# Performance work log

Measured on AMD Instinct MI355X. Metric: run time of the kernel, lower is better.

Reference implementation:

```python
import jax, jax.numpy as jnp
import numpy as np

N_NODES = 100000
AVG_DEG = 16
D_IN, D_HID, D_OUT = 128, 128, 64


def setup_inputs() -> dict:
    key = jax.random.key(0)
    k_x, k_w1, k_w2 = jax.random.split(key, 3)
    rng = np.random.default_rng(0)
    # random adjacency edges + self-loops (I + A)
    src = rng.integers(0, N_NODES, N_NODES * AVG_DEG)
    dst = rng.integers(0, N_NODES, N_NODES * AVG_DEG)
    loops = np.arange(N_NODES)
    src = np.concatenate([src, loops]).astype(np.int32)
    dst = np.concatenate([dst, loops]).astype(np.int32)
    # symmetric normalization D^{-1/2} (I+A) D^{-1/2}; deg = row sums of I+A
    deg = np.bincount(src, minlength=N_NODES).astype(np.float32)
    val = (1.0 / np.sqrt(deg[src] * deg[dst])).astype(np.float32)
    return {
        "x": jax.random.normal(k_x, (N_NODES, D_IN), dtype=jnp.float32),
        "W1": jax.random.normal(k_w1, (D_IN, D_HID), dtype=jnp.float32),
        "W2": jax.random.normal(k_w2, (D_HID, D_OUT), dtype=jnp.float32),
        "edge_src": jnp.asarray(src),
        "edge_dst": jnp.asarray(dst),
        "edge_val": jnp.asarray(val),
    }


def _gcn_layer(x, W, src, dst, val, n):
    xw = x @ W                               # dense GEMM: [N, d_out]
    msg = val[:, None] * xw[dst]             # gather along edges: [E, d_out]
    return jax.ops.segment_sum(msg, src, num_segments=n)  # A_hat @ (XW)


def reference(x, W1, W2, edge_src, edge_dst, edge_val):
    n = x.shape[0]
    h = jax.nn.relu(_gcn_layer(x, W1, edge_src, edge_dst, edge_val, n))
    h = jax.nn.relu(_gcn_layer(h, W2, edge_src, edge_dst, edge_val, n))
    return jax.nn.softmax(h, axis=-1)
```

## Files before the change

### kernel.cpp

```cpp
#include <hip/hip_runtime.h>
#include <hip/hip_fp16.h>
#include <math.h>

#define DHID 128
#define DOUT 64
#define EPB 4096
#define BUCK_SH 8

typedef _Float16 half8 __attribute__((ext_vector_type(8)));
typedef float f32x4 __attribute__((ext_vector_type(4)));

static inline size_t align_up(size_t v, size_t a) { return (v + a - 1) / a * a; }


__global__ __launch_bounds__(256) void k_bincount(const int* __restrict__ src, int* __restrict__ dir,
                                                  int* __restrict__ btot, int E, int nbuck, int nblka) {
    __shared__ int hist[512];
    int tid = threadIdx.x;
    for (int i = tid; i < nbuck; i += 256) hist[i] = 0;
    __syncthreads();
    int e0 = blockIdx.x * EPB;
    #pragma unroll
    for (int j = 0; j < EPB / 256; ++j) {
        int e = e0 + tid + j * 256;
        if (e < E) atomicAdd(&hist[src[e] >> BUCK_SH], 1);
    }
    __syncthreads();
    for (int i = tid; i < nbuck; i += 256) {
        int c = hist[i];
        dir[i * nblka + blockIdx.x] = c;
        if (c) atomicAdd(&btot[i], c);
    }
}

__global__ __launch_bounds__(256) void k_dirscan(int* __restrict__ dir, const int* __restrict__ btot,
                                                 int* __restrict__ bucketbase, int* __restrict__ off,
                                                 int n, int nbuck, int nblka, int E) {
    __shared__ int h[512], s4[128], redb[256];
    int tid = threadIdx.x, b = blockIdx.x;
    int s = 0;
    for (int i = tid; i < b; i += 256) s += btot[i];
    redb[tid] = s; __syncthreads();
    #pragma unroll
    for (int d = 128; d > 0; d >>= 1) {
        if (tid < d) redb[tid] += redb[tid + d];
        __syncthreads();
    }
    int base = redb[0];
    if (tid == 0) {
        bucketbase[b] = base;
        if (b == 0) off[n] = E;
        if (b == nbuck - 1) bucketbase[nbuck] = E;
    }
    for (int j = tid; j < nblka; j += 256) h[j] = dir[b * nblka + j];
    __syncthreads();
    int nq = (nblka + 3) >> 2;
    if (tid < nq) {
        int t = 0;
        #pragma unroll
        for (int j = 0; j < 4; ++j) { int idx = tid * 4 + j; if (idx < nblka) t += h[idx]; }
        s4[tid] = t;
    }
    __syncthreads();
    if (tid == 0) { int run = 0; for (int i = 0; i < nq; ++i) { int t = s4[i]; s4[i] = run; run += t; } }
    __syncthreads();
    if (tid < nq) {
        int run = s4[tid] + base;
        #pragma unroll
        for (int j = 0; j < 4; ++j) {
            int idx = tid * 4 + j;
            if (idx < nblka) { int t = h[idx]; dir[b * nblka + idx] = run; run += t; }
        }
    }
}

__global__ __launch_bounds__(256) void k_binwrite(const int* __restrict__ src, const int* __restrict__ dst,
                                                  const float* __restrict__ val, const int* __restrict__ dir,
                                                  int2* __restrict__ ctmp, int E, int nbuck, int nblka) {
    __shared__ int cur[512];
    int tid = threadIdx.x, blk = blockIdx.x;
    for (int i = tid; i < nbuck; i += 256) cur[i] = dir[i * nblka + blk];
    __syncthreads();
    int e0 = blk * EPB;
    #pragma unroll
    for (int j = 0; j < EPB / 256; ++j) {
        int e = e0 + tid + j * 256;
        if (e < E) {
            int s = src[e];
            int bk = s >> BUCK_SH;
            int p = atomicAdd(&cur[bk], 1);
            ctmp[p] = make_int2(((s & 255) << 17) | dst[e], __float_as_int(val[e]));
        }
    }
}

__global__ __launch_bounds__(256) void k_csrify(const int* __restrict__ bucketbase,
                                                const int2* __restrict__ ctmp, int2* __restrict__ cpair,
                                                int* __restrict__ off, int n) {
    __shared__ int h[256], loff[256], cur[256], s4[64];
    int tid = threadIdx.x, b = blockIdx.x;
    int base = bucketbase[b];
    int cnt = bucketbase[b + 1] - base;
    h[tid] = 0;
    __syncthreads();
    for (int i = tid; i < cnt; i += 256) atomicAdd(&h[ctmp[base + i].x >> 17], 1);
    __syncthreads();
    if (tid < 64) {
        int s = 0;
        #pragma unroll
        for (int j = 0; j < 4; ++j) s += h[tid * 4 + j];
        s4[tid] = s;
    }
    __syncthreads();
    if (tid == 0) { int run = 0; for (int i = 0; i < 64; ++i) { int t = s4[i]; s4[i] = run; run += t; } }
    __syncthreads();
    if (tid < 64) {
        int run = s4[tid];
        #pragma unroll
        for (int j = 0; j < 4; ++j) { int idx = tid * 4 + j; loff[idx] = run; run += h[idx]; }
    }
    __syncthreads();
    int node0 = b << BUCK_SH;
    int nodes_b = n - node0; if (nodes_b > 256) nodes_b = 256;
    if (tid < nodes_b) off[node0 + tid] = base + loff[tid];
    cur[tid] = loff[tid];
    __syncthreads();
    for (int i = tid; i < cnt; i += 256) {
        int2 v = ctmp[base + i];
        int sl = v.x >> 17;
        int p = atomicAdd(&cur[sl], 1);
        cpair[base + p] = make_int2(v.x & 0x1FFFF, v.y);
    }
}

__global__ __launch_bounds__(256) void k_wprep(const float* __restrict__ W1, const float* __restrict__ W2,
                                               _Float16* __restrict__ Wt1, _Float16* __restrict__ Wt2,
                                               int* __restrict__ btot, int nbuck) {
    int b = blockIdx.x, tid = threadIdx.x;
    int gid = b * 256 + tid;
    if (gid < nbuck) btot[gid] = 0;
    if (b < 64) {
        int m = b * 256 + tid;
        int c = m >> 7, k = m & 127;
        Wt1[m] = (_Float16)W1[(size_t)k * 128 + c];
    } else {
        int m = (b - 64) * 256 + tid;
        int c = m >> 7, k = m & 127;
        Wt2[m] = (_Float16)W2[(size_t)k * 64 + c];
    }
}

__global__ __launch_bounds__(256) void k_gemm1(const float* __restrict__ x, const _Float16* __restrict__ Wt1,
                                               __half* __restrict__ xw, int n) {
    __shared__ _Float16 Ws[128 * 128];
    int tid = threadIdx.x;
    int row0 = blockIdx.x * 64;

    #pragma unroll
    for (int m0 = 0; m0 < 2048; m0 += 256) {
        int m = tid + m0;
        int c = m >> 4, kq = m & 15;
        uint4 v = *(const uint4*)(Wt1 + (size_t)m * 8);
        int byte = (c * 256 + kq * 16) ^ ((c & 7) << 4);
        *(uint4*)((char*)Ws + byte) = v;
    }
    __syncthreads();

    int lane = tid & 63;
    int wid = tid >> 6;
    int rg = row0 + wid * 16 + (lane & 15); if (rg >= n) rg = n - 1;
    int kgrp = (lane >> 4) * 8;

    f32x4 acc[8];
    #pragma unroll
    for (int t = 0; t < 8; ++t) acc[t] = (f32x4){0.f, 0.f, 0.f, 0.f};

    #pragma unroll
    for (int kk = 0; kk < 128; kk += 32) {
        int ks = kk + kgrp;
        const float4* xp = (const float4*)(x + (size_t)rg * 128 + ks);
        float4 f0 = xp[0], f1 = xp[1];
        half8 a;
        a[0] = (_Float16)f0.x; a[1] = (_Float16)f0.y; a[2] = (_Float16)f0.z; a[3] = (_Float16)f0.w;
        a[4] = (_Float16)f1.x; a[5] = (_Float16)f1.y; a[6] = (_Float16)f1.z; a[7] = (_Float16)f1.w;
        #pragma unroll
        for (int t = 0; t < 8; ++t) {
            int c = t * 16 + (lane & 15);
            int bbyte = (c * 256 + ks * 2) ^ ((c & 7) << 4);
            half8 b = *(const half8*)((const char*)Ws + bbyte);
            acc[t] = __builtin_amdgcn_mfma_f32_16x16x32_f16(a, b, acc[t], 0, 0, 0);
        }
    }

    #pragma unroll
    for (int t = 0; t < 8; ++t) {
        int c = t * 16 + (lane & 15);
        #pragma unroll
        for (int j = 0; j < 4; ++j) {
            int rs = row0 + wid * 16 + (lane >> 4) * 4 + j;
            if (rs < n) xw[(size_t)rs * 128 + c] = __float2half(acc[t][j]);
        }
    }
}

__global__ __launch_bounds__(256) void k_gemm2(const __half* __restrict__ h1, const _Float16* __restrict__ Wt2,
                                               __half* __restrict__ hw, int n) {
    __shared__ _Float16 Ws[64 * 128];
    int tid = threadIdx.x;
    int row0 = blockIdx.x * 64;

    #pragma unroll
    for (int m0 = 0; m0 < 1024; m0 += 256) {
        int m = tid + m0;
        int c = m >> 4, kq = m & 15;
        uint4 v = *(const uint4*)(Wt2 + (size_t)m * 8);
        int byte = (c * 256 + kq * 16) ^ ((c & 7) << 4);
        *(uint4*)((char*)Ws + byte) = v;
    }
    __syncthreads();

    int lane = tid & 63;
    int wid = tid >> 6;
    int rg = row0 + wid * 16 + (lane & 15); if (rg >= n) rg = n - 1;
    int kgrp = (lane >> 4) * 8;

    f32x4 acc[4];
    #pragma unroll
    for (int t = 0; t < 4; ++t) acc[t] = (f32x4){0.f, 0.f, 0.f, 0.f};

    #pragma unroll
    for (int kk = 0; kk < 128; kk += 32) {
        int ks = kk + kgrp;
        half8 a = *(const half8*)((const void*)(h1 + (size_t)rg * 128 + ks));
        #pragma unroll
        for (int t = 0; t < 4; ++t) {
            int c = t * 16 + (lane & 15);
            int bbyte = (c * 256 + ks * 2) ^ ((c & 7) << 4);
            half8 b = *(const half8*)((const char*)Ws + bbyte);
            acc[t] = __builtin_amdgcn_mfma_f32_16x16x32_f16(a, b, acc[t], 0, 0, 0);
        }
    }

    #pragma unroll
    for (int t = 0; t < 4; ++t) {
        int c = t * 16 + (lane & 15);
        #pragma unroll
        for (int j = 0; j < 4; ++j) {
            int rs = row0 + wid * 16 + (lane >> 4) * 4 + j;
            if (rs < n) hw[(size_t)rs * 64 + c] = __float2half(acc[t][j]);
        }
    }
}

__global__ __launch_bounds__(256) void k_agg1(const __half* __restrict__ xw, const int* __restrict__ off,
                                              const int2* __restrict__ cpair,
                                              __half* __restrict__ h1, int n) {
    int wave = threadIdx.x >> 6;
    int lane = threadIdx.x & 63;
    int node = blockIdx.x * 4 + wave;
    if (node >= n) return;
    int s = off[node], e = off[node + 1];
    float ax = 0.f, ay = 0.f;
    int i = s;
    for (; i + 8 <= e; i += 8) {
        int2 p[8];
        #pragma unroll
        for (int j = 0; j < 8; ++j) p[j] = cpair[i + j];
        float2 v[8];
        #pragma unroll
        for (int j = 0; j < 8; ++j)
            v[j] = __half22float2(((const __half2*)(xw + (size_t)p[j].x * 128))[lane]);
        #pragma unroll
        for (int j = 0; j < 8; ++j) {
            float w = __int_as_float(p[j].y);
            ax += w * v[j].x; ay += w * v[j].y;
        }
    }
    for (; i + 4 <= e; i += 4) {
        int2 p[4];
        #pragma unroll
        for (int j = 0; j < 4; ++j) p[j] = cpair[i + j];
        float2 v[4];
        #pragma unroll
        for (int j = 0; j < 4; ++j)
            v[j] = __half22float2(((const __half2*)(xw + (size_t)p[j].x * 128))[lane]);
        #pragma unroll
        for (int j = 0; j < 4; ++j) {
            float w = __int_as_float(p[j].y);
            ax += w * v[j].x; ay += w * v[j].y;
        }
    }
    for (; i < e; ++i) {
        int2 p = cpair[i];
        float w = __int_as_float(p.y);
        float2 v = __half22float2(((const __half2*)(xw + (size_t)p.x * 128))[lane]);
        ax += w * v.x; ay += w * v.y;
    }
    ((__half2*)(h1 + (size_t)node * 128))[lane] = __floats2half2_rn(fmaxf(ax, 0.f), fmaxf(ay, 0.f));
}

__global__ __launch_bounds__(256) void k_agg2(const __half* __restrict__ hw, const int* __restrict__ off,
                                              const int2* __restrict__ cpair,
                                              float* __restrict__ out, int n) {
    int wave = threadIdx.x >> 6;
    int lane = threadIdx.x & 63;
    int node = blockIdx.x * 4 + wave;
    if (node >= n) return;
    int s = off[node], e = off[node + 1];
    float acc = 0.f;
    int i = s;
    for (; i + 8 <= e; i += 8) {
        int2 p[8];
        #pragma unroll
        for (int j = 0; j < 8; ++j) p[j] = cpair[i + j];
        float v[8];
        #pragma unroll
        for (int j = 0; j < 8; ++j)
            v[j] = __half2float(hw[(size_t)p[j].x * 64 + lane]);
        #pragma unroll
        for (int j = 0; j < 8; ++j)
            acc += __int_as_float(p[j].y) * v[j];
    }
    for (; i + 4 <= e; i += 4) {
        int2 p[4];
        #pragma unroll
        for (int j = 0; j < 4; ++j) p[j] = cpair[i + j];
        float v[4];
        #pragma unroll
        for (int j = 0; j < 4; ++j)
            v[j] = __half2float(hw[(size_t)p[j].x * 64 + lane]);
        #pragma unroll
        for (int j = 0; j < 4; ++j)
            acc += __int_as_float(p[j].y) * v[j];
    }
    for (; i < e; ++i) {
        int2 p = cpair[i];
        acc += __int_as_float(p.y) * __half2float(hw[(size_t)p.x * 64 + lane]);
    }
    acc = fmaxf(acc, 0.f);
    float m = acc;
    #pragma unroll
    for (int o = 32; o > 0; o >>= 1) m = fmaxf(m, __shfl_xor(m, o));
    float ex = expf(acc - m);
    float sum = ex;
    #pragma unroll
    for (int o = 32; o > 0; o >>= 1) sum += __shfl_xor(sum, o);
    out[(size_t)node * 64 + lane] = ex / sum;
}

extern "C" void kernel_launch(void* const* d_in, const int* in_sizes, int n_in,
                              void* d_out, int out_size, void* d_ws, size_t ws_size,
                              hipStream_t stream) {
    const float* x = (const float*)d_in[0];
    const float* W1 = (const float*)d_in[1];
    const float* W2 = (const float*)d_in[2];
    const int* esrc = (const int*)d_in[3];
    const int* edst = (const int*)d_in[4];
    const float* evalv = (const float*)d_in[5];
    int n = in_sizes[0] / DHID;
    int E = in_sizes[3];

    int nbuck = (n + 255) >> BUCK_SH;
    int nblka = (E + EPB - 1) / EPB;

    char* p = (char*)d_ws;
    int* off = (int*)p;        p += align_up((size_t)(n + 1) * 4, 256);
    int* bucketbase = (int*)p; p += align_up((size_t)(nbuck + 1) * 4, 256);
    int* btot = (int*)p;       p += align_up((size_t)nbuck * 4, 256);
    int* dir = (int*)p;        p += align_up((size_t)nbuck * nblka * 4, 256);
    int2* ctmp = (int2*)p;     p += align_up((size_t)E * 8, 256);
    int2* cpair = (int2*)p;    p += align_up((size_t)E * 8, 256);
    _Float16* Wt1 = (_Float16*)p; p += align_up((size_t)128 * 128 * 2, 256);
    _Float16* Wt2 = (_Float16*)p; p += align_up((size_t)64 * 128 * 2, 256);
    __half* xw = (__half*)p;   p += align_up((size_t)n * DHID * 2, 256);
    __half* h1 = (__half*)p;   p += align_up((size_t)n * DHID * 2, 256);
    __half* hw2 = xw;

    k_wprep<<<96, 256, 0, stream>>>(W1, W2, Wt1, Wt2, btot, nbuck);
    k_gemm1<<<(n + 63) / 64, 256, 0, stream>>>(x, Wt1, xw, n);
    k_bincount<<<nblka, 256, 0, stream>>>(esrc, dir, btot, E, nbuck, nblka);
    k_dirscan<<<nbuck, 256, 0, stream>>>(dir, btot, bucketbase, off, n, nbuck, nblka, E);
    k_binwrite<<<nblka, 256, 0, stream>>>(esrc, edst, evalv, dir, ctmp, E, nbuck, nblka);
    k_csrify<<<nbuck, 256, 0, stream>>>(bucketbase, ctmp, cpair, off, n);
    k_agg1<<<(n + 3) / 4, 256, 0, stream>>>(xw, off, cpair, h1, n);
    k_gemm2<<<(n + 63) / 64, 256, 0, stream>>>(h1, Wt2, hw2, n);
    k_agg2<<<(n + 3) / 4, 256, 0, stream>>>(hw2, off, cpair, (float*)d_out, n);
}
```

Measured before the change: 212.3 us.

## Slice layer-1 features into column panels for cache-local aggregation

The GEMM1 output and the layer-1 hidden activations are stored as eight column slices of 16 halves (32 bytes) per node instead of a row-major 256-byte row. Layer-1 aggregation now launches eight times as many blocks, one per slice. Each wave splits a node's edges across eight lane groups and combines them with shuffles, so each slice's working set (about 3.2 MB) can stay in L2 or the MALL. Edge-pair loads use nontemporal hints in both aggregations. The cost is that the edge list is reread eight times in layer 1, the gathers are narrower, and there is extra shuffle-reduction work.

```diff
diff --git a/kernel.cpp b/kernel.cpp
--- a/kernel.cpp
+++ b/kernel.cpp
@@ -151,7 +151,7 @@
 }
 
 __global__ __launch_bounds__(256) void k_gemm1(const float* __restrict__ x, const _Float16* __restrict__ Wt1,
-                                               __half* __restrict__ xw, int n) {
+                                               __half* __restrict__ xw_s, int n) {
     __shared__ _Float16 Ws[128 * 128];
     int tid = threadIdx.x;
     int row0 = blockIdx.x * 64;
@@ -194,16 +194,15 @@
 
     #pragma unroll
     for (int t = 0; t < 8; ++t) {
-        int c = t * 16 + (lane & 15);
         #pragma unroll
         for (int j = 0; j < 4; ++j) {
             int rs = row0 + wid * 16 + (lane >> 4) * 4 + j;
-            if (rs < n) xw[(size_t)rs * 128 + c] = __float2half(acc[t][j]);
-        }
-    }
-}
-
-__global__ __launch_bounds__(256) void k_gemm2(const __half* __restrict__ h1, const _Float16* __restrict__ Wt2,
+            if (rs < n) xw_s[((size_t)t * n + rs) * 16 + (lane & 15)] = __float2half(acc[t][j]);
+        }
+    }
+}
+
+__global__ __launch_bounds__(256) void k_gemm2(const __half* __restrict__ h1_s, const _Float16* __restrict__ Wt2,
                                                __half* __restrict__ hw, int n) {
     __shared__ _Float16 Ws[64 * 128];
     int tid = threadIdx.x;
@@ -231,7 +230,8 @@
     #pragma unroll
     for (int kk = 0; kk < 128; kk += 32) {
         int ks = kk + kgrp;
-        half8 a = *(const half8*)((const void*)(h1 + (size_t)rg * 128 + ks));
+        const __half* aptr = h1_s + ((size_t)(ks >> 4) * n + rg) * 16 + (ks & 15);
+        half8 a = *(const half8*)((const void*)aptr);
         #pragma unroll
         for (int t = 0; t < 4; ++t) {
             int c = t * 16 + (lane & 15);
@@ -252,51 +252,31 @@
     }
 }
 
-__global__ __launch_bounds__(256) void k_agg1(const __half* __restrict__ xw, const int* __restrict__ off,
+__global__ __launch_bounds__(256) void k_agg1(const __half* __restrict__ xw_s, const int* __restrict__ off,
                                               const int2* __restrict__ cpair,
-                                              __half* __restrict__ h1, int n) {
-    int wave = threadIdx.x >> 6;
+                                              __half* __restrict__ h1_s, int n) {
+    int slice = blockIdx.x & 7;
+    int node = (blockIdx.x >> 3) * 4 + (threadIdx.x >> 6);
+    if (node >= n) return;
     int lane = threadIdx.x & 63;
-    int node = blockIdx.x * 4 + wave;
-    if (node >= n) return;
+    int l = lane & 7;
+    int g = lane >> 3;
     int s = off[node], e = off[node + 1];
+    const __half2* base = (const __half2*)(xw_s + (size_t)slice * n * 16);
     float ax = 0.f, ay = 0.f;
-    int i = s;
-    for (; i + 8 <= e; i += 8) {
-        int2 p[8];
-        #pragma unroll
-        for (int j = 0; j < 8; ++j) p[j] = cpair[i + j];
-        float2 v[8];
-        #pragma unroll
-        for (int j = 0; j < 8; ++j)
-            v[j] = __half22float2(((const __half2*)(xw + (size_t)p[j].x * 128))[lane]);
-        #pragma unroll
-        for (int j = 0; j < 8; ++j) {
-            float w = __int_as_float(p[j].y);
-            ax += w * v[j].x; ay += w * v[j].y;
-        }
-    }
-    for (; i + 4 <= e; i += 4) {
-        int2 p[4];
-        #pragma unroll
-        for (int j = 0; j < 4; ++j) p[j] = cpair[i + j];
-        float2 v[4];
-        #pragma unroll
-        for (int j = 0; j < 4; ++j)
-            v[j] = __half22float2(((const __half2*)(xw + (size_t)p[j].x * 128))[lane]);
-        #pragma unroll
-        for (int j = 0; j < 4; ++j) {
-            float w = __int_as_float(p[j].y);
-            ax += w * v[j].x; ay += w * v[j].y;
-        }
-    }
-    for (; i < e; ++i) {
-        int2 p = cpair[i];
-        float w = __int_as_float(p.y);
-        float2 v = __half22float2(((const __half2*)(xw + (size_t)p.x * 128))[lane]);
+    for (int i = s + g; i < e; i += 8) {
+        long long pk = __builtin_nontemporal_load((const long long*)(cpair + i));
+        int dst = (int)(pk & 0xFFFFFFFFLL);
+        float w = __int_as_float((int)(pk >> 32));
+        float2 v = __half22float2(base[(size_t)dst * 8 + l]);
         ax += w * v.x; ay += w * v.y;
     }
-    ((__half2*)(h1 + (size_t)node * 128))[lane] = __floats2half2_rn(fmaxf(ax, 0.f), fmaxf(ay, 0.f));
+    #pragma unroll
+    for (int o = 8; o < 64; o <<= 1) { ax += __shfl_xor(ax, o); ay += __shfl_xor(ay, o); }
+    if (g == 0) {
+        ((__half2*)(h1_s + ((size_t)slice * n + node) * 16))[l] =
+            __floats2half2_rn(fmaxf(ax, 0.f), fmaxf(ay, 0.f));
+    }
 }
 
 __global__ __launch_bounds__(256) void k_agg2(const __half* __restrict__ hw, const int* __restrict__ off,
@@ -310,32 +290,33 @@
     float acc = 0.f;
     int i = s;
     for (; i + 8 <= e; i += 8) {
-        int2 p[8];
-        #pragma unroll
-        for (int j = 0; j < 8; ++j) p[j] = cpair[i + j];
+        long long pk[8];
+        #pragma unroll
+        for (int j = 0; j < 8; ++j) pk[j] = __builtin_nontemporal_load((const long long*)(cpair + i + j));
         float v[8];
         #pragma unroll
         for (int j = 0; j < 8; ++j)
-            v[j] = __half2float(hw[(size_t)p[j].x * 64 + lane]);
+            v[j] = __half2float(hw[(size_t)(int)(pk[j] & 0xFFFFFFFFLL) * 64 + lane]);
         #pragma unroll
         for (int j = 0; j < 8; ++j)
-            acc += __int_as_float(p[j].y) * v[j];
+            acc += __int_as_float((int)(pk[j] >> 32)) * v[j];
     }
     for (; i + 4 <= e; i += 4) {
-        int2 p[4];
-        #pragma unroll
-        for (int j = 0; j < 4; ++j) p[j] = cpair[i + j];
+        long long pk[4];
+        #pragma unroll
+        for (int j = 0; j < 4; ++j) pk[j] = __builtin_nontemporal_load((const long long*)(cpair + i + j));
         float v[4];
         #pragma unroll
         for (int j = 0; j < 4; ++j)
-            v[j] = __half2float(hw[(size_t)p[j].x * 64 + lane]);
+            v[j] = __half2float(hw[(size_t)(int)(pk[j] & 0xFFFFFFFFLL) * 64 + lane]);
         #pragma unroll
         for (int j = 0; j < 4; ++j)
-            acc += __int_as_float(p[j].y) * v[j];
+            acc += __int_as_float((int)(pk[j] >> 32)) * v[j];
     }
     for (; i < e; ++i) {
-        int2 p = cpair[i];
-        acc += __int_as_float(p.y) * __half2float(hw[(size_t)p.x * 64 + lane]);
+        long long pk = __builtin_nontemporal_load((const long long*)(cpair + i));
+        acc += __int_as_float((int)(pk >> 32)) *
+               __half2float(hw[(size_t)(int)(pk & 0xFFFFFFFFLL) * 64 + lane]);
     }
     acc = fmaxf(acc, 0.f);
     float m = acc;
@@ -382,7 +363,7 @@
     k_dirscan<<<nbuck, 256, 0, stream>>>(dir, btot, bucketbase, off, n, nbuck, nblka, E);
     k_binwrite<<<nblka, 256, 0, stream>>>(esrc, edst, evalv, dir, ctmp, E, nbuck, nblka);
     k_csrify<<<nbuck, 256, 0, stream>>>(bucketbase, ctmp, cpair, off, n);
-    k_agg1<<<(n + 3) / 4, 256, 0, stream>>>(xw, off, cpair, h1, n);
+    k_agg1<<<((n + 3) / 4) * 8, 256, 0, stream>>>(xw, off, cpair, h1, n);
     k_gemm2<<<(n + 63) / 64, 256, 0, stream>>>(h1, Wt2, hw2, n);
     k_agg2<<<(n + 3) / 4, 256, 0, stream>>>(hw2, off, cpair, (float*)d_out, n);
 }
```

Result: slower. 452.6 us (+113.2%).
